# Kernel optimization log

Hardware: AMD Instinct MI355X
Metric: run time of the kernel (lower is better)

## Reference

```python
import jax, jax.numpy as jnp
import numpy as np

L, B, E, H, NH = 128, 32, 128, 256, 8
NUM_NODE, ETA = 20000, 100


def setup_inputs() -> dict:
    key = jax.random.key(0)
    ks = jax.random.split(key, 24)
    s = 0.05
    rn = lambda k, sh: jax.random.normal(k, sh, dtype=jnp.float32) * s
    return {
        "node": jax.random.randint(ks[0], (L, B), 0, NUM_NODE + 1),
        "ts": jax.random.normal(ks[1], (L, B, 2), dtype=jnp.float32),
        "seq_lengths": jnp.sort(jax.random.randint(ks[2], (B,), 64, L + 1))[::-1],
        "embed_table": rn(ks[3], (NUM_NODE + 1, E)),
        "Wih0": rn(ks[4], (3 * H, E + 2)), "Whh0": rn(ks[5], (3 * H, H)),
        "bih0": rn(ks[6], (3 * H,)), "bhh0": rn(ks[7], (3 * H,)),
        "Wih1": rn(ks[8], (3 * H, H)), "Whh1": rn(ks[9], (3 * H, H)),
        "bih1": rn(ks[10], (3 * H,)), "bhh1": rn(ks[11], (3 * H,)),
        "Wa0": rn(ks[12], (E, 2 * E)), "ba0": rn(ks[13], (E,)),
        "Wa1": rn(ks[14], (NH, E)), "ba1": rn(ks[15], (NH,)),
        "Wf0": rn(ks[16], (168, H * (NH + 1))), "bf0": rn(ks[17], (168,)),
        "Wf1": rn(ks[18], (ETA, 168)), "bf1": rn(ks[19], (ETA,)),
    }


def gru_layer(x, Wih, Whh, bih, bhh, lengths):
    # x: [L, B, in]; PyTorch GRU cell, with pack/pad semantics:
    # hidden frozen and output zeroed for t >= length (emulates pack_padded_sequence).
    Lx, Bx, _ = x.shape

    def step(h, xs):
        x_t, t = xs
        gi = x_t @ Wih.T + bih          # [B, 3H]
        gh = h @ Whh.T + bhh            # [B, 3H]
        ir, iz, in_ = jnp.split(gi, 3, axis=-1)
        hr, hz, hn = jnp.split(gh, 3, axis=-1)
        r = jax.nn.sigmoid(ir + hr)
        z = jax.nn.sigmoid(iz + hz)
        n = jnp.tanh(in_ + r * hn)
        h_new = (1.0 - z) * n + z * h
        valid = (t < lengths)[:, None]
        h = jnp.where(valid, h_new, h)
        return h, jnp.where(valid, h_new, jnp.zeros_like(h_new))

    h0 = jnp.zeros((Bx, Whh.shape[1]), x.dtype)
    hT, outs = jax.lax.scan(step, h0, (x, jnp.arange(Lx)))
    return outs, hT


def reference(node, ts, seq_lengths, embed_table,
              Wih0, Whh0, bih0, bhh0, Wih1, Whh1, bih1, bhh1,
              Wa0, ba0, Wa1, ba1, Wf0, bf0, Wf1, bf1):
    e = embed_table[node]                          # [L, B, E]
    embeds = jnp.concatenate([e, ts], axis=-1)     # [L, B, E+2]

    # pairwise attention: a[i,j] = e[j], b[i,j] = e[i] (repeat + transpose)
    a = jnp.broadcast_to(e[None], (L, L, B, E))
    b = jnp.broadcast_to(e[:, None], (L, L, B, E))
    pair = jnp.concatenate([a, b], axis=-1)        # [L, L, B, 2E]
    hid = jax.nn.relu(pair @ Wa0.T + ba0)          # [L, L, B, E]
    w = (hid @ Wa1.T + ba1).sum(axis=1)            # [L, B, NH]

    # multiplicative length mask, then softmax over time axis (as in original)
    mask = (jnp.arange(L)[:, None] < seq_lengths[None, :]).astype(w.dtype)[..., None]
    w = jax.nn.softmax(w * mask, axis=0)           # [L, B, NH]

    out0, _ = gru_layer(embeds, Wih0, Whh0, bih0, bhh0, seq_lengths)
    out1, hT = gru_layer(out0, Wih1, Whh1, bih1, bhh1, seq_lengths)  # [L,B,H], [B,H]

    ctx = jnp.einsum('lbh,lbd->bhd', w, out1).reshape(B, NH * H)     # [B, NH*H]
    z = jnp.concatenate([ctx, hT], axis=-1) @ Wf0.T + bf0
    z = jax.nn.selu(z)
    logits = z @ Wf1.T + bf1
    return jax.nn.log_softmax(logits, axis=-1)
```

## Files before the change

### kernel.cpp

```cpp
#include <hip/hip_runtime.h>
#include <hip/hip_bf16.h>

#define LL 128
#define BB 32
#define EE 128
#define HH 256
#define NHH 8
#define G3 768
#define IN0 130
#define ETA 100
#define F1 168
#define CLSIN 2304

typedef _Float16 half_t;
typedef __attribute__((ext_vector_type(2))) _Float16 half2v;

#if defined(__has_builtin)
#if __has_builtin(__builtin_amdgcn_fdot2)
#define HAVE_FDOT2 1
#endif
#endif

__device__ __forceinline__ float fdot2f(half2v a, half2v b, float c) {
#ifdef HAVE_FDOT2
  return __builtin_amdgcn_fdot2(a, b, c, false);
#else
  return c + (float)a.x * (float)b.x + (float)a.y * (float)b.y;
#endif
}
__device__ __forceinline__ float fdot2u(unsigned int a, unsigned int b, float c) {
  return fdot2f(__builtin_bit_cast(half2v, a), __builtin_bit_cast(half2v, b), c);
}

#define BARRIER_LDS() __asm__ volatile("s_waitcnt lgkmcnt(0)\n\ts_barrier" ::: "memory")

__device__ __forceinline__ float sigmoidf_(float x) { return 1.0f / (1.0f + __expf(-x)); }
__device__ __forceinline__ float tanhf_(float x) { return 1.0f - 2.0f / (__expf(2.0f * x) + 1.0f); }

__global__ void prep_kernel(
    const float* __restrict__ Wa0, const float* __restrict__ Wih0,
    const float* __restrict__ Wih1, const float* __restrict__ Whh0,
    const float* __restrict__ Whh1,
    half_t* __restrict__ Wa0Ta, half_t* __restrict__ Wa0Tb,
    half2v* __restrict__ Wih0T2, half2v* __restrict__ Wih1T2,
    half_t* __restrict__ Whh0h, half_t* __restrict__ Whh1h)
{
  int idx = blockIdx.x * blockDim.x + threadIdx.x;
  const int n1 = 16384, n2 = 16384, n3 = 65 * 768, n4 = 128 * 768, n5 = 196608;
  if (idx < n1) {
    int d = idx >> 7, k = idx & 127;
    Wa0Ta[idx] = (half_t)Wa0[k * 256 + d];
  } else if ((idx -= n1) < n2) {
    int d = idx >> 7, k = idx & 127;
    Wa0Tb[idx] = (half_t)Wa0[k * 256 + 128 + d];
  } else if ((idx -= n2) < n3) {
    int d2 = idx / 768, r = idx % 768;
    half2v w; w.x = (half_t)Wih0[r * IN0 + 2 * d2]; w.y = (half_t)Wih0[r * IN0 + 2 * d2 + 1];
    Wih0T2[idx] = w;
  } else if ((idx -= n3) < n4) {
    int d2 = idx / 768, r = idx % 768;
    half2v w; w.x = (half_t)Wih1[r * HH + 2 * d2]; w.y = (half_t)Wih1[r * HH + 2 * d2 + 1];
    Wih1T2[idx] = w;
  } else if ((idx -= n4) < n5) {
    Whh0h[idx] = (half_t)Whh0[idx];
  } else if ((idx -= n5) < n5) {
    Whh1h[idx] = (half_t)Whh1[idx];
  }
}

__global__ void embed_uv_kernel(
    const int* __restrict__ node,
    const float* __restrict__ table,
    const half_t* __restrict__ Wa0Ta,
    const half_t* __restrict__ Wa0Tb,
    const float* __restrict__ ba0,
    half2v* __restrict__ e_h2,
    float* __restrict__ U,
    float* __restrict__ V)
{
  int lb = blockIdx.x;
  int k = threadIdx.x;
  __shared__ float es[EE];
  int n = node[lb];
  float ev = table[(size_t)n * EE + k];
  es[k] = ev;
  __syncthreads();
  if (k < 64) {
    half2v p; p.x = (half_t)es[2 * k]; p.y = (half_t)es[2 * k + 1];
    e_h2[(size_t)lb * 64 + k] = p;
  }
  float u = 0.f, v = ba0[k];
  #pragma unroll 8
  for (int d = 0; d < EE; ++d) {
    float x = es[d];
    u += (float)Wa0Ta[d * EE + k] * x;
    v += (float)Wa0Tb[d * EE + k] * x;
  }
  U[(size_t)lb * EE + k] = u;
  V[(size_t)lb * EE + k] = v;
}

__global__ __launch_bounds__(128) void attn_w_kernel(
    const float* __restrict__ U, const float* __restrict__ V,
    const float* __restrict__ Wa1,
    const float* __restrict__ ba1,
    float* __restrict__ wpre)
{
  int ig = blockIdx.x >> 5;
  int b = blockIdx.x & 31;
  int i0 = ig * 4;
  int k = threadIdx.x;
  float vk[4];
  #pragma unroll
  for (int ii = 0; ii < 4; ++ii) vk[ii] = V[((size_t)(i0 + ii) * BB + b) * EE + k];
  float wa[NHH], acc[4][NHH];
  #pragma unroll
  for (int h = 0; h < NHH; ++h) wa[h] = Wa1[h * EE + k];
  #pragma unroll
  for (int ii = 0; ii < 4; ++ii)
    #pragma unroll
    for (int h = 0; h < NHH; ++h) acc[ii][h] = 0.f;
  for (int j = 0; j < LL; ++j) {
    float u = U[((size_t)j * BB + b) * EE + k];
    #pragma unroll
    for (int ii = 0; ii < 4; ++ii) {
      float tv = fmaxf(u + vk[ii], 0.f);
      #pragma unroll
      for (int h = 0; h < NHH; ++h) acc[ii][h] += wa[h] * tv;
    }
  }
  __shared__ float part[2][32];
  int wave = k >> 6, lane = k & 63;
  #pragma unroll
  for (int ii = 0; ii < 4; ++ii)
    #pragma unroll
    for (int h = 0; h < NHH; ++h) {
      float a = acc[ii][h];
      #pragma unroll
      for (int off = 32; off > 0; off >>= 1) a += __shfl_xor(a, off, 64);
      if (lane == 0) part[wave][ii * 8 + h] = a;
    }
  __syncthreads();
  if (k < 32) {
    int ii = k >> 3, h = k & 7;
    float w = part[0][k] + part[1][k] + (float)LL * ba1[h];
    wpre[((size_t)(i0 + ii) * BB + b) * NHH + h] = w;
  }
}

__global__ void attn_softmax_kernel(
    const float* __restrict__ wpre, const int* __restrict__ slen,
    float* __restrict__ wsoft)
{
  int b = blockIdx.x >> 3;
  int h = blockIdx.x & 7;
  int l = threadIdx.x;
  int len = slen[b];
  float x = wpre[((size_t)l * BB + b) * NHH + h];
  float xv = (l < len) ? x : 0.f;
  float m = xv;
  #pragma unroll
  for (int off = 32; off > 0; off >>= 1) m = fmaxf(m, __shfl_xor(m, off, 64));
  __shared__ float sm[2], ss[2];
  int wave = l >> 6;
  if ((l & 63) == 0) sm[wave] = m;
  __syncthreads();
  m = fmaxf(sm[0], sm[1]);
  float e = __expf(xv - m);
  float s = e;
  #pragma unroll
  for (int off = 32; off > 0; off >>= 1) s += __shfl_xor(s, off, 64);
  if ((l & 63) == 0) ss[wave] = s;
  __syncthreads();
  s = ss[0] + ss[1];
  wsoft[((size_t)l * BB + b) * NHH + h] = e / s;
}

__global__ __launch_bounds__(256) void gi0_kernel(
    const half2v* __restrict__ e_h2, const float* __restrict__ ts,
    const half2v* __restrict__ W2,
    const float* __restrict__ bih,
    float* __restrict__ gi)
{
  int lb0 = blockIdx.x * 8;
  int tid = threadIdx.x;
  __shared__ half2v xs2[8][66];
  for (int idx = tid; idx < 512; idx += 256) {
    int q = idx >> 6, d2 = idx & 63;
    xs2[q][d2] = e_h2[(size_t)(lb0 + q) * 64 + d2];
  }
  if (tid < 8) {
    half2v t2; t2.x = (half_t)ts[(lb0 + tid) * 2]; t2.y = (half_t)ts[(lb0 + tid) * 2 + 1];
    xs2[tid][64] = t2;
  }
  __syncthreads();
  float acc[8][3];
  #pragma unroll
  for (int q = 0; q < 8; ++q) { acc[q][0] = 0.f; acc[q][1] = 0.f; acc[q][2] = 0.f; }
  for (int d2 = 0; d2 < 65; ++d2) {
    half2v w0 = W2[d2 * 768 + tid];
    half2v w1 = W2[d2 * 768 + 256 + tid];
    half2v w2 = W2[d2 * 768 + 512 + tid];
    #pragma unroll
    for (int q = 0; q < 8; ++q) {
      half2v x = xs2[q][d2];
      acc[q][0] = fdot2f(w0, x, acc[q][0]);
      acc[q][1] = fdot2f(w1, x, acc[q][1]);
      acc[q][2] = fdot2f(w2, x, acc[q][2]);
    }
  }
  float b0 = bih[tid], b1 = bih[256 + tid], b2 = bih[512 + tid];
  #pragma unroll
  for (int q = 0; q < 8; ++q) {
    float* gp = gi + (size_t)(lb0 + q) * G3;
    gp[tid] = acc[q][0] + b0; gp[256 + tid] = acc[q][1] + b1; gp[512 + tid] = acc[q][2] + b2;
  }
}

__global__ __launch_bounds__(256) void gi1_kernel(
    const float* __restrict__ out0,
    const half2v* __restrict__ W2,
    const float* __restrict__ bih,
    float* __restrict__ gi)
{
  int lb0 = blockIdx.x * 8;
  int tid = threadIdx.x;
  __shared__ half2v xs2[8][128];
  for (int idx = tid; idx < 1024; idx += 256) {
    int q = idx >> 7, d2 = idx & 127;
    float2 v = ((const float2*)(out0 + (size_t)(lb0 + q) * HH))[d2];
    half2v x; x.x = (half_t)v.x; x.y = (half_t)v.y;
    xs2[q][d2] = x;
  }
  __syncthreads();
  float acc[8][3];
  #pragma unroll
  for (int q = 0; q < 8; ++q) { acc[q][0] = 0.f; acc[q][1] = 0.f; acc[q][2] = 0.f; }
  for (int d2 = 0; d2 < 128; ++d2) {
    half2v w0 = W2[d2 * 768 + tid];
    half2v w1 = W2[d2 * 768 + 256 + tid];
    half2v w2 = W2[d2 * 768 + 512 + tid];
    #pragma unroll
    for (int q = 0; q < 8; ++q) {
      half2v x = xs2[q][d2];
      acc[q][0] = fdot2f(w0, x, acc[q][0]);
      acc[q][1] = fdot2f(w1, x, acc[q][1]);
      acc[q][2] = fdot2f(w2, x, acc[q][2]);
    }
  }
  float b0 = bih[tid], b1 = bih[256 + tid], b2 = bih[512 + tid];
  #pragma unroll
  for (int q = 0; q < 8; ++q) {
    float* gp = gi + (size_t)(lb0 + q) * G3;
    gp[tid] = acc[q][0] + b0; gp[256 + tid] = acc[q][1] + b1; gp[512 + tid] = acc[q][2] + b2;
  }
}

__global__ __launch_bounds__(512, 2) void gru_scan_kernel(
    const half_t* __restrict__ Whhh,
    const float* __restrict__ bhh,
    const float* __restrict__ gi,
    const int* __restrict__ slen,
    float* __restrict__ out,
    float* __restrict__ hT)
{
  const int b = blockIdx.x;
  const int tid = threadIdx.x;
  const int s = tid & 3;
  const int g = tid >> 2;
  __shared__ __align__(16) uint4 h4[4 * 9];
  __shared__ float p5[768 * 5];

  unsigned int wRegU[192];
  #pragma unroll
  for (int r = 0; r < 6; ++r) {
    const uint4* wp = (const uint4*)(Whhh + (size_t)(6 * g + r) * HH + 64 * s);
    #pragma unroll
    for (int j = 0; j < 8; ++j) {
      uint4 v = wp[j];
      wRegU[r * 32 + 4 * j + 0] = v.x; wRegU[r * 32 + 4 * j + 1] = v.y;
      wRegU[r * 32 + 4 * j + 2] = v.z; wRegU[r * 32 + 4 * j + 3] = v.w;
    }
  }
  #pragma unroll
  for (int i = 0; i < 192; ++i) __asm__ volatile("" : "+v"(wRegU[i]));

  const int len = slen[b];
  float bhr = 0.f, bhz = 0.f, bhn = 0.f, hold = 0.f;
  if (tid < HH) {
    bhr = bhh[tid]; bhz = bhh[HH + tid]; bhn = bhh[2 * HH + tid];
  }
  if (tid < 36) { uint4 z; z.x = z.y = z.z = z.w = 0u; h4[tid] = z; }
  __syncthreads();

  const float* gib = gi + (size_t)b * G3;
  float* outb = out + (size_t)b * HH;

  #pragma unroll 1
  for (int t = 0; t < LL; ++t) {
    float g0 = 0.f, g1 = 0.f, g2 = 0.f;
    if (tid < HH) {
      const float* gp = gib + (size_t)t * (BB * G3);
      g0 = gp[tid]; g1 = gp[HH + tid]; g2 = gp[2 * HH + tid];
    }
    float acc[6] = {0.f, 0.f, 0.f, 0.f, 0.f, 0.f};
    #pragma unroll
    for (int c = 0; c < 4; ++c) {
      uint4 ha = h4[s * 9 + 2 * c];
      uint4 hb = h4[s * 9 + 2 * c + 1];
      unsigned int hu[8] = {ha.x, ha.y, ha.z, ha.w, hb.x, hb.y, hb.z, hb.w};
      #pragma unroll
      for (int r = 0; r < 6; ++r) {
        #pragma unroll
        for (int i = 0; i < 8; ++i)
          acc[r] = fdot2u(wRegU[r * 32 + 8 * c + i], hu[i], acc[r]);
      }
    }
    #pragma unroll
    for (int r = 0; r < 6; ++r)
      p5[(6 * g + r) * 5 + s] = acc[r];
    BARRIER_LDS();
    if (tid < HH) {
      int b0 = tid * 5, b1 = (HH + tid) * 5, b2 = (2 * HH + tid) * 5;
      float srz = (p5[b0] + p5[b0 + 1]) + (p5[b0 + 2] + p5[b0 + 3]);
      float sz  = (p5[b1] + p5[b1 + 1]) + (p5[b1 + 2] + p5[b1 + 3]);
      float sn  = (p5[b2] + p5[b2 + 1]) + (p5[b2 + 2] + p5[b2 + 3]);
      float r_ = sigmoidf_(g0 + srz + bhr);
      float z_ = sigmoidf_(g1 + sz + bhz);
      float n_ = tanhf_(g2 + r_ * (sn + bhn));
      float hnew = (1.f - z_) * n_ + z_ * hold;
      bool valid = t < len;
      hold = valid ? hnew : hold;
      ((half_t*)(h4 + (tid >> 6) * 9))[tid & 63] = (half_t)hold;
      outb[(size_t)t * (BB * HH) + tid] = valid ? hnew : 0.f;
    }
    BARRIER_LDS();
  }
  if (tid < HH) hT[(size_t)b * HH + tid] = hold;
}

__global__ void ctx_kernel(
    const float* __restrict__ wsoft, const float* __restrict__ out1,
    float* __restrict__ ctx)
{
  int b = blockIdx.x >> 3, h = blockIdx.x & 7;
  int d = threadIdx.x;
  float acc = 0.f;
  for (int l = 0; l < LL; ++l) {
    float w = wsoft[((size_t)l * BB + b) * NHH + h];
    acc += w * out1[((size_t)l * BB + b) * HH + d];
  }
  ctx[(size_t)b * (NHH * HH) + h * HH + d] = acc;
}

__global__ __launch_bounds__(512) void final_kernel(
    const float* __restrict__ ctx, const float* __restrict__ hT,
    const float* __restrict__ Wf0,
    const float* __restrict__ bf0,
    const float* __restrict__ Wf1,
    const float* __restrict__ bf1,
    float* __restrict__ outp)
{
  int b = blockIdx.x;
  int tid = threadIdx.x;
  int wave = tid >> 6, lane = tid & 63;
  __shared__ float4 xs4[CLSIN / 4];
  __shared__ float zs[F1];
  __shared__ float ls[ETA];
  float* xs = (float*)xs4;
  for (int i = tid; i < NHH * HH; i += 512) xs[i] = ctx[(size_t)b * (NHH * HH) + i];
  if (tid < HH) xs[NHH * HH + tid] = hT[(size_t)b * HH + tid];
  __syncthreads();
  for (int r = wave; r < F1; r += 8) {
    const float4* wp = (const float4*)(Wf0 + (size_t)r * CLSIN);
    float acc = 0.f;
    #pragma unroll
    for (int i = 0; i < CLSIN / 4 / 64; ++i) {
      float4 w = wp[lane + 64 * i];
      float4 x = xs4[lane + 64 * i];
      acc += w.x * x.x + w.y * x.y + w.z * x.z + w.w * x.w;
    }
    #pragma unroll
    for (int off = 32; off > 0; off >>= 1) acc += __shfl_xor(acc, off, 64);
    if (lane == 0) {
      float x = acc + bf0[r];
      const float alpha = 1.6732632423543772f, scale = 1.0507009873554805f;
      zs[r] = scale * (x > 0.f ? x : alpha * (__expf(x) - 1.f));
    }
  }
  __syncthreads();
  for (int r = wave; r < ETA; r += 8) {
    float acc = 0.f;
    for (int k = lane; k < F1; k += 64) acc += Wf1[r * F1 + k] * zs[k];
    #pragma unroll
    for (int off = 32; off > 0; off >>= 1) acc += __shfl_xor(acc, off, 64);
    if (lane == 0) ls[r] = acc + bf1[r];
  }
  __syncthreads();
  if (wave == 0) {
    float v0 = (lane < ETA) ? ls[lane] : -1e30f;
    float v1 = (lane + 64 < ETA) ? ls[lane + 64] : -1e30f;
    float m = fmaxf(v0, v1);
    #pragma unroll
    for (int off = 32; off > 0; off >>= 1) m = fmaxf(m, __shfl_xor(m, off, 64));
    float s = __expf(v0 - m) + __expf(v1 - m);
    #pragma unroll
    for (int off = 32; off > 0; off >>= 1) s += __shfl_xor(s, off, 64);
    float lse = m + __logf(s);
    if (lane < ETA) outp[(size_t)b * ETA + lane] = v0 - lse;
    if (lane + 64 < ETA) outp[(size_t)b * ETA + lane + 64] = v1 - lse;
  }
}

extern "C" void kernel_launch(void* const* d_in, const int* in_sizes, int n_in,
                              void* d_out, int out_size, void* d_ws, size_t ws_size,
                              hipStream_t stream) {
  const int*   node  = (const int*)d_in[0];
  const float* ts    = (const float*)d_in[1];
  const int*   slen  = (const int*)d_in[2];
  const float* table = (const float*)d_in[3];
  const float* Wih0  = (const float*)d_in[4];
  const float* Whh0  = (const float*)d_in[5];
  const float* bih0  = (const float*)d_in[6];
  const float* bhh0  = (const float*)d_in[7];
  const float* Wih1  = (const float*)d_in[8];
  const float* Whh1  = (const float*)d_in[9];
  const float* bih1  = (const float*)d_in[10];
  const float* bhh1  = (const float*)d_in[11];
  const float* Wa0   = (const float*)d_in[12];
  const float* ba0   = (const float*)d_in[13];
  const float* Wa1   = (const float*)d_in[14];
  const float* ba1   = (const float*)d_in[15];
  const float* Wf0   = (const float*)d_in[16];
  const float* bf0   = (const float*)d_in[17];
  const float* Wf1   = (const float*)d_in[18];
  const float* bf1   = (const float*)d_in[19];

  char* ws = (char*)d_ws;
  size_t off = 0;
  auto alloc = [&](size_t n) { void* p = (void*)(ws + off); off += (n + 255) & ~(size_t)255; return p; };

  half2v* e_h2 = (half2v*)alloc((size_t)LL * BB * 64 * 4);
  float* U     = (float*)alloc((size_t)LL * BB * EE * 4);
  float* V     = (float*)alloc((size_t)LL * BB * EE * 4);
  float* gi    = (float*)alloc((size_t)LL * BB * G3 * 4);
  float* out0  = (float*)alloc((size_t)LL * BB * HH * 4);
  float* out1  = (float*)alloc((size_t)LL * BB * HH * 4);
  float* hTb   = (float*)alloc((size_t)BB * HH * 4);
  float* wpre  = (float*)alloc((size_t)LL * BB * NHH * 4);
  float* wsoft = (float*)alloc((size_t)LL * BB * NHH * 4);
  float* ctxb  = (float*)alloc((size_t)BB * NHH * HH * 4);
  half_t* Wa0Ta = (half_t*)alloc((size_t)128 * 128 * 2);
  half_t* Wa0Tb = (half_t*)alloc((size_t)128 * 128 * 2);
  half2v* Wih0T2 = (half2v*)alloc((size_t)65 * 768 * 4);
  half2v* Wih1T2 = (half2v*)alloc((size_t)128 * 768 * 4);
  half_t* Whh0h = (half_t*)alloc((size_t)G3 * HH * 2);
  half_t* Whh1h = (half_t*)alloc((size_t)G3 * HH * 2);
  if (off > ws_size) return;

  const int prep_total = 16384 + 16384 + 65 * 768 + 128 * 768 + 196608 + 196608;
  prep_kernel<<<(prep_total + 255) / 256, 256, 0, stream>>>(
      Wa0, Wih0, Wih1, Whh0, Whh1, Wa0Ta, Wa0Tb, Wih0T2, Wih1T2, Whh0h, Whh1h);
  embed_uv_kernel<<<LL * BB, 128, 0, stream>>>(node, table, Wa0Ta, Wa0Tb, ba0, e_h2, U, V);
  attn_w_kernel<<<(LL / 4) * BB, 128, 0, stream>>>(U, V, Wa1, ba1, wpre);
  attn_softmax_kernel<<<BB * NHH, 128, 0, stream>>>(wpre, slen, wsoft);
  gi0_kernel<<<LL * BB / 8, 256, 0, stream>>>(e_h2, ts, Wih0T2, bih0, gi);
  gru_scan_kernel<<<BB, 512, 0, stream>>>(Whh0h, bhh0, gi, slen, out0, hTb);
  gi1_kernel<<<LL * BB / 8, 256, 0, stream>>>(out0, Wih1T2, bih1, gi);
  gru_scan_kernel<<<BB, 512, 0, stream>>>(Whh1h, bhh1, gi, slen, out1, hTb);
  ctx_kernel<<<BB * NHH, 256, 0, stream>>>(wsoft, out1, ctxb);
  final_kernel<<<BB, 512, 0, stream>>>(ctxb, hTb, Wf0, bf0, Wf1, bf1, (float*)d_out);
}
```

Baseline: 590.9 us.

## Halve GRU scan block to 256 threads with 384 weight registers each

```diff
diff --git a/kernel.cpp b/kernel.cpp
--- a/kernel.cpp
+++ b/kernel.cpp
@@ -256,7 +256,7 @@
   }
 }
 
-__global__ __launch_bounds__(512, 2) void gru_scan_kernel(
+__global__ __launch_bounds__(256, 1) void gru_scan_kernel(
     const half_t* __restrict__ Whhh,
     const float* __restrict__ bhh,
     const float* __restrict__ gi,
@@ -266,31 +266,23 @@
 {
   const int b = blockIdx.x;
   const int tid = threadIdx.x;
-  const int s = tid & 3;
-  const int g = tid >> 2;
-  __shared__ __align__(16) uint4 h4[4 * 9];
-  __shared__ float p5[768 * 5];
-
-  unsigned int wRegU[192];
+  const int s = tid & 1;
+  const int g = tid >> 1;
+  __shared__ __align__(16) uint4 h4[2][17];
+  __shared__ float p3[768 * 3];
+
+  uint4 w[96];
   #pragma unroll
   for (int r = 0; r < 6; ++r) {
-    const uint4* wp = (const uint4*)(Whhh + (size_t)(6 * g + r) * HH + 64 * s);
-    #pragma unroll
-    for (int j = 0; j < 8; ++j) {
-      uint4 v = wp[j];
-      wRegU[r * 32 + 4 * j + 0] = v.x; wRegU[r * 32 + 4 * j + 1] = v.y;
-      wRegU[r * 32 + 4 * j + 2] = v.z; wRegU[r * 32 + 4 * j + 3] = v.w;
-    }
-  }
-  #pragma unroll
-  for (int i = 0; i < 192; ++i) __asm__ volatile("" : "+v"(wRegU[i]));
+    const uint4* wp = (const uint4*)(Whhh + (size_t)(6 * g + r) * HH + 128 * s);
+    #pragma unroll
+    for (int j = 0; j < 16; ++j) w[r * 16 + j] = wp[j];
+  }
 
   const int len = slen[b];
-  float bhr = 0.f, bhz = 0.f, bhn = 0.f, hold = 0.f;
-  if (tid < HH) {
-    bhr = bhh[tid]; bhz = bhh[HH + tid]; bhn = bhh[2 * HH + tid];
-  }
-  if (tid < 36) { uint4 z; z.x = z.y = z.z = z.w = 0u; h4[tid] = z; }
+  float bhr = bhh[tid], bhz = bhh[HH + tid], bhn = bhh[2 * HH + tid];
+  float hold = 0.f;
+  if (tid < 34) { uint4 z; z.x = z.y = z.z = z.w = 0u; ((uint4*)h4)[tid] = z; }
   __syncthreads();
 
   const float* gib = gi + (size_t)b * G3;
@@ -298,45 +290,41 @@
 
   #pragma unroll 1
   for (int t = 0; t < LL; ++t) {
-    float g0 = 0.f, g1 = 0.f, g2 = 0.f;
-    if (tid < HH) {
-      const float* gp = gib + (size_t)t * (BB * G3);
-      g0 = gp[tid]; g1 = gp[HH + tid]; g2 = gp[2 * HH + tid];
-    }
+    const float* gp = gib + (size_t)t * (BB * G3);
+    float g0 = gp[tid], g1 = gp[HH + tid], g2 = gp[2 * HH + tid];
     float acc[6] = {0.f, 0.f, 0.f, 0.f, 0.f, 0.f};
     #pragma unroll
-    for (int c = 0; c < 4; ++c) {
-      uint4 ha = h4[s * 9 + 2 * c];
-      uint4 hb = h4[s * 9 + 2 * c + 1];
-      unsigned int hu[8] = {ha.x, ha.y, ha.z, ha.w, hb.x, hb.y, hb.z, hb.w};
+    for (int c = 0; c < 16; ++c) {
+      uint4 hv = h4[s][c];
       #pragma unroll
       for (int r = 0; r < 6; ++r) {
-        #pragma unroll
-        for (int i = 0; i < 8; ++i)
-          acc[r] = fdot2u(wRegU[r * 32 + 8 * c + i], hu[i], acc[r]);
+        uint4 wv = w[r * 16 + c];
+        acc[r] = fdot2u(wv.x, hv.x, acc[r]);
+        acc[r] = fdot2u(wv.y, hv.y, acc[r]);
+        acc[r] = fdot2u(wv.z, hv.z, acc[r]);
+        acc[r] = fdot2u(wv.w, hv.w, acc[r]);
       }
     }
     #pragma unroll
     for (int r = 0; r < 6; ++r)
-      p5[(6 * g + r) * 5 + s] = acc[r];
+      p3[(6 * g + r) * 3 + s] = acc[r];
     BARRIER_LDS();
-    if (tid < HH) {
-      int b0 = tid * 5, b1 = (HH + tid) * 5, b2 = (2 * HH + tid) * 5;
-      float srz = (p5[b0] + p5[b0 + 1]) + (p5[b0 + 2] + p5[b0 + 3]);
-      float sz  = (p5[b1] + p5[b1 + 1]) + (p5[b1 + 2] + p5[b1 + 3]);
-      float sn  = (p5[b2] + p5[b2 + 1]) + (p5[b2 + 2] + p5[b2 + 3]);
+    {
+      float srz = p3[tid * 3] + p3[tid * 3 + 1];
+      float sz  = p3[(HH + tid) * 3] + p3[(HH + tid) * 3 + 1];
+      float sn  = p3[(2 * HH + tid) * 3] + p3[(2 * HH + tid) * 3 + 1];
       float r_ = sigmoidf_(g0 + srz + bhr);
       float z_ = sigmoidf_(g1 + sz + bhz);
       float n_ = tanhf_(g2 + r_ * (sn + bhn));
       float hnew = (1.f - z_) * n_ + z_ * hold;
       bool valid = t < len;
       hold = valid ? hnew : hold;
-      ((half_t*)(h4 + (tid >> 6) * 9))[tid & 63] = (half_t)hold;
+      ((half_t*)(h4[tid >> 7]))[tid & 127] = (half_t)hold;
       outb[(size_t)t * (BB * HH) + tid] = valid ? hnew : 0.f;
     }
     BARRIER_LDS();
   }
-  if (tid < HH) hT[(size_t)b * HH + tid] = hold;
+  hT[(size_t)b * HH + tid] = hold;
 }
 
 __global__ void ctx_kernel(
@@ -465,9 +453,9 @@
   attn_w_kernel<<<(LL / 4) * BB, 128, 0, stream>>>(U, V, Wa1, ba1, wpre);
   attn_softmax_kernel<<<BB * NHH, 128, 0, stream>>>(wpre, slen, wsoft);
   gi0_kernel<<<LL * BB / 8, 256, 0, stream>>>(e_h2, ts, Wih0T2, bih0, gi);
-  gru_scan_kernel<<<BB, 512, 0, stream>>>(Whh0h, bhh0, gi, slen, out0, hTb);
+  gru_scan_kernel<<<BB, 256, 0, stream>>>(Whh0h, bhh0, gi, slen, out0, hTb);
   gi1_kernel<<<LL * BB / 8, 256, 0, stream>>>(out0, Wih1T2, bih1, gi);
-  gru_scan_kernel<<<BB, 512, 0, stream>>>(Whh1h, bhh1, gi, slen, out1, hTb);
+  gru_scan_kernel<<<BB, 256, 0, stream>>>(Whh1h, bhh1, gi, slen, out1, hTb);
   ctx_kernel<<<BB * NHH, 256, 0, stream>>>(wsoft, out1, ctxb);
   final_kernel<<<BB, 512, 0, stream>>>(ctxb, hTb, Wf0, bf0, Wf1, bf1, (float*)d_out);
 }
```

Result: slower. 787.5 us (+33.3%).
